# Kernel optimization log

Measured on AMD Instinct MI355X. Metric: run time of the kernel, lower is better.

## Reference

```python
import jax, jax.numpy as jnp
import numpy as np
from jax import lax

SIGMA = 4
TOPK = 9
GRID = 28          # patch grid hardcoded in AnomalyMapGenerator
IMG = 224          # input_size
SCALE = IMG // GRID  # nearest-neighbor upsample factor = 8
KSIZE = 2 * int(4.0 * SIGMA + 0.5) + 1  # 33, as in compute_anomaly_map


def _gaussian_kernel1d():
    x = jnp.arange(KSIZE, dtype=jnp.float32) - KSIZE // 2
    g = jnp.exp(-(x * x) / (2.0 * SIGMA * SIGMA))
    return g / jnp.sum(g)


def _gaussian_blur2d(x):
    # x: [B,1,H,W]; separable gaussian with reflect padding (kornia default)
    g = _gaussian_kernel1d()
    pad = KSIZE // 2
    # blur along H
    xh = jnp.pad(x, ((0, 0), (0, 0), (pad, pad), (0, 0)), mode='reflect')
    xh = lax.conv_general_dilated(xh, g.reshape(1, 1, KSIZE, 1), (1, 1), 'VALID')
    # blur along W
    xw = jnp.pad(xh, ((0, 0), (0, 0), (0, 0), (pad, pad)), mode='reflect')
    return lax.conv_general_dilated(xw, g.reshape(1, 1, 1, KSIZE), (1, 1), 'VALID')


def setup_inputs() -> dict:
    key = jax.random.key(0)
    k1, k2 = jax.random.split(key)
    embedding = jax.random.normal(k1, (3136, 1536), dtype=jnp.float32)
    memory_bank = jax.random.normal(k2, (20000, 1536), dtype=jnp.float32)  # M x D
    return {"embedding": embedding, "memory_bank": memory_bank}


def reference(embedding, memory_bank):
    x2 = jnp.sum(embedding * embedding, axis=-1, keepdims=True)        # [N,1]
    y2 = jnp.sum(memory_bank * memory_bank, axis=-1)                   # [M]
    d2 = x2 + y2[None, :] - 2.0 * (embedding @ memory_bank.T)          # [N,M]
    dist = jnp.sqrt(jnp.maximum(d2, 0.0))
    # topk smallest, ascending (matches torch.topk largest=False)
    neg_top, _ = lax.top_k(-dist, TOPK)
    patch_scores = -neg_top                                            # [N,9]

    # --- compute_anomaly_map ---
    batch = patch_scores.shape[0] // (GRID * GRID)
    amap = patch_scores[:, 0].reshape(batch, 1, GRID, GRID)
    # F.interpolate default mode='nearest' with integer factor 8 == repeat
    amap = jnp.repeat(jnp.repeat(amap, SCALE, axis=2), SCALE, axis=3)  # [B,1,224,224]
    amap = _gaussian_blur2d(amap)

    # --- compute_anomaly_score ---
    idx = jnp.argmax(patch_scores[:, 0])
    confidence = patch_scores[idx]                                     # [9]
    e = jnp.exp(confidence)
    weights = 1.0 - jnp.max(e) / jnp.sum(e)
    score = weights * jnp.max(patch_scores[:, 0])
    return amap, score
```

## Files before the change

### kernel.cpp

```cpp
#include <hip/hip_runtime.h>

typedef __attribute__((ext_vector_type(4))) int i32x4;

#define N_ROWS 3136
#define M_COLS 20000
#define KDIM   1536
#define NCT    157
#define NRT    25
#define NWG    (NCT * NRT)
#define PPR    (NCT*9)

#define QSCL   (4.0f / 127.0f)
#define QINV   (127.0f / 4.0f)
#define TWO_S2 (2.0f * QSCL * QSCL)

#define GLOAD_LDS16(g, l) __builtin_amdgcn_global_load_lds( \
    (const __attribute__((address_space(1))) unsigned int*)(g), \
    (__attribute__((address_space(3))) unsigned int*)(l), 16, 0, 0)

__device__ inline void t9_insert(float (&t)[9], float v) {
    #pragma unroll
    for (int s = 8; s >= 1; --s)
        t[s] = __builtin_amdgcn_fmed3f(v, t[s-1], t[s]);
    t[0] = fminf(t[0], v);
}

__device__ inline int q8(float x) {
    int q = (int)rintf(x * QINV);
    q = q > 127 ? 127 : q;
    q = q < -127 ? -127 : q;
    return q & 255;
}

__global__ void cvt_norm_kernel(const float* __restrict__ emb,
                                const float* __restrict__ mb,
                                unsigned char* __restrict__ embq,
                                unsigned char* __restrict__ mbq,
                                float* __restrict__ x2, float* __restrict__ y2) {
    int lane = threadIdx.x & 63;
    int row = blockIdx.x * (blockDim.x >> 6) + (threadIdx.x >> 6);
    const float* src; unsigned char* dst; float* nrm; int r;
    if (row < M_COLS) { src = mb;  dst = mbq;  nrm = y2; r = row; }
    else              { src = emb; dst = embq; nrm = x2; r = row - M_COLS; }
    const float4* p = (const float4*)(src + (size_t)r * KDIM);
    int* q = (int*)(dst + (size_t)r * KDIM);
    float s = 0.f;
    #pragma unroll
    for (int i = 0; i < 6; ++i) {
        float4 v = p[lane + i * 64];
        s += v.x*v.x + v.y*v.y + v.z*v.z + v.w*v.w;
        q[lane + i * 64] = q8(v.x) | (q8(v.y) << 8) | (q8(v.z) << 16) | (q8(v.w) << 24);
    }
    #pragma unroll
    for (int off = 32; off > 0; off >>= 1) s += __shfl_down(s, off);
    if (lane == 0) nrm[r] = s;
}

union SMem {
    unsigned char stg[2][16384];
    struct { float Ds[32 * 129]; float T9[8 * 32 * 9]; } epi;
};

#define STAGE(BUF, KT) do { \
    const int koff_ = (KT) * 64; \
    GLOAD_LDS16(pa[0] + koff_, sm.stg[BUF] + ldsoff[0]); \
    GLOAD_LDS16(pa[1] + koff_, sm.stg[BUF] + ldsoff[1]); \
    GLOAD_LDS16(pb[0] + koff_, sm.stg[BUF] + 8192 + ldsoff[0]); \
    GLOAD_LDS16(pb[1] + koff_, sm.stg[BUF] + 8192 + ldsoff[1]); \
} while (0)

#define KSTEP(CB, NB, KT, PF) do { \
    if (PF) STAGE(NB, (KT) + 1); \
    i32x4 af[4], bfr[4]; \
    _Pragma("unroll") \
    for (int mi = 0; mi < 4; ++mi) \
        af[mi] = *(const i32x4*)(sm.stg[CB] + (wr + mi * 16 + l15) * 64 + kbs); \
    _Pragma("unroll") \
    for (int ni = 0; ni < 4; ++ni) \
        bfr[ni] = *(const i32x4*)(sm.stg[CB] + 8192 + (wc + ni * 16 + l15) * 64 + kbs); \
    _Pragma("unroll") \
    for (int mi = 0; mi < 4; ++mi) \
        _Pragma("unroll") \
        for (int ni = 0; ni < 4; ++ni) \
            acc[mi][ni] = __builtin_amdgcn_mfma_i32_16x16x64_i8(af[mi], bfr[ni], acc[mi][ni], 0, 0, 0); \
    asm volatile("s_waitcnt vmcnt(0)" ::: "memory"); \
    __builtin_amdgcn_s_barrier(); \
} while (0)

__global__ __launch_bounds__(256, 4) void dist_topk_kernel(
    const unsigned char* __restrict__ Aq,
    const unsigned char* __restrict__ Bq,
    const float* __restrict__ x2, const float* __restrict__ y2,
    float* __restrict__ partials)
{
    __shared__ __align__(16) SMem sm;

    const int tid = threadIdx.x;
    const int wave = tid >> 6, lane = tid & 63;

    int orig = blockIdx.x;
    int xcd = orig & 7, li = orig >> 3;
    const int qc = NWG / 8, rc = NWG % 8;
    int wg = (xcd < rc ? xcd * (qc + 1) : rc * (qc + 1) + (xcd - rc) * qc) + li;
    const int ct = wg / NRT, rt = wg % NRT;
    const int rowBase = rt * 128, colBase = ct * 128;

    const unsigned char* pa[2];
    const unsigned char* pb[2];
    int ldsoff[2];
    #pragma unroll
    for (int i = 0; i < 2; ++i) {
        int flat = i * 256 + tid;
        int r = flat >> 2;
        int kk = (((flat & 3) ^ ((flat >> 3) & 3))) * 16;
        int ar = rowBase + r; ar = ar < N_ROWS ? ar : N_ROWS - 1;
        int bc = colBase + r; bc = bc < M_COLS ? bc : M_COLS - 1;
        pa[i] = Aq + (size_t)ar * KDIM + kk;
        pb[i] = Bq + (size_t)bc * KDIM + kk;
        ldsoff[i] = flat * 16;
    }

    const int l15 = lane & 15;
    const int kb = (lane >> 4) * 16;
    const int kbs = kb ^ (((l15 >> 1) & 3) << 4);
    const int g4 = (lane >> 4) * 4;
    const int wr = (wave >> 1) * 64;
    const int wc = (wave & 1) * 64;

    i32x4 acc[4][4] = {};

    STAGE(0, 0);
    asm volatile("s_waitcnt vmcnt(0)" ::: "memory");
    __builtin_amdgcn_s_barrier();

    #pragma unroll 1
    for (int kt = 0; kt < 24; kt += 2) {
        KSTEP(0, 1, kt, 1);
        KSTEP(1, 0, kt + 1, (kt + 2) < 24);
    }

    int ncols = M_COLS - colBase; ncols = ncols < 128 ? ncols : 128;

    #pragma unroll
    for (int p = 0; p < 4; ++p) {
        __syncthreads();
        if ((wave >> 1) == (p >> 1)) {
            const int mi0 = (p & 1) * 2;
            #pragma unroll
            for (int ni = 0; ni < 4; ++ni) {
                int c = wc + ni * 16 + l15;
                int gc = colBase + c;
                float yv = y2[gc < M_COLS ? gc : M_COLS - 1];
                #pragma unroll
                for (int mh = 0; mh < 2; ++mh) {
                    #pragma unroll
                    for (int j = 0; j < 4; ++j) {
                        int rloc = mh * 16 + g4 + j;
                        int gr = rowBase + p * 32 + rloc;
                        float xv = x2[gr < N_ROWS ? gr : N_ROWS - 1];
                        sm.epi.Ds[rloc * 129 + c] = xv + yv - TWO_S2 * (float)acc[mi0 + mh][ni][j];
                    }
                }
            }
        }
        __syncthreads();
        int r = tid & 31, q8g = tid >> 5;
        int grow = rowBase + p * 32 + r;
        float t9[9];
        #pragma unroll
        for (int s = 0; s < 9; ++s) t9[s] = 3.4e38f;
        int cs = q8g * 16;
        int ce = (cs + 16 < ncols) ? cs + 16 : ncols;
        for (int c = cs; c < ce; ++c) t9_insert(t9, sm.epi.Ds[r * 129 + c]);
        #pragma unroll
        for (int s = 0; s < 9; ++s) sm.epi.T9[(q8g * 32 + r) * 9 + s] = t9[s];
        __syncthreads();
        if (q8g < 4) {
            #pragma unroll
            for (int s = 0; s < 9; ++s)
                t9_insert(t9, sm.epi.T9[((q8g + 4) * 32 + r) * 9 + s]);
            #pragma unroll
            for (int s = 0; s < 9; ++s) sm.epi.T9[(q8g * 32 + r) * 9 + s] = t9[s];
        }
        __syncthreads();
        if (q8g == 0 && grow < N_ROWS) {
            #pragma unroll
            for (int qq = 1; qq < 4; ++qq)
                #pragma unroll
                for (int s = 0; s < 9; ++s)
                    t9_insert(t9, sm.epi.T9[(qq * 32 + r) * 9 + s]);
            float* dst = partials + (size_t)grow * PPR + ct * 9;
            #pragma unroll
            for (int s = 0; s < 9; ++s) dst[s] = t9[s];
        }
    }
}

__global__ void merge_topk_kernel(const float* __restrict__ partials,
                                  float* __restrict__ scores) {
    int lane = threadIdx.x & 63;
    int row = blockIdx.x * 4 + (threadIdx.x >> 6);
    const float* p = partials + (size_t)row * PPR;
    float t9[9];
    #pragma unroll
    for (int s = 0; s < 9; ++s) t9[s] = 3.4e38f;
    for (int i = lane; i < PPR; i += 64) {
        float v = p[i];
        if (v < t9[8]) t9_insert(t9, v);
    }
    #pragma unroll
    for (int off = 32; off > 0; off >>= 1) {
        float o[9];
        #pragma unroll
        for (int s = 0; s < 9; ++s) o[s] = __shfl_xor(t9[s], off);
        #pragma unroll
        for (int s = 0; s < 9; ++s)
            if (o[s] < t9[8]) t9_insert(t9, o[s]);
    }
    if (lane == 0) {
        #pragma unroll
        for (int s = 0; s < 9; ++s)
            scores[row * 9 + s] = sqrtf(fmaxf(t9[s], 0.f));
    }
}

__global__ void blur_h_kernel(const float* __restrict__ scores, float* __restrict__ tH) {
    int idx = blockIdx.x * blockDim.x + threadIdx.x;
    if (idx >= 4 * 224 * 28) return;
    int pw = idx % 28, y = (idx / 28) % 224, b = idx / (28 * 224);
    float acc = 0.f, gsum = 0.f;
    #pragma unroll
    for (int k = 0; k < 33; ++k) {
        float xk = (float)(k - 16);
        float w = expf(-xk * xk * (1.0f / 32.0f));
        gsum += w;
        int yy = y - 16 + k;
        yy = yy < 0 ? -yy : yy;
        yy = yy > 223 ? 446 - yy : yy;
        acc += w * scores[(size_t)(b * 784 + (yy >> 3) * 28 + pw) * 9];
    }
    tH[idx] = acc / gsum;
}

__global__ void blur_w_kernel(const float* __restrict__ tH, float* __restrict__ out) {
    int idx = blockIdx.x * blockDim.x + threadIdx.x;
    if (idx >= 4 * 224 * 224) return;
    int x = idx % 224, y = (idx / 224) % 224, b = idx / (224 * 224);
    float acc = 0.f, gsum = 0.f;
    #pragma unroll
    for (int k = 0; k < 33; ++k) {
        float xk = (float)(k - 16);
        float w = expf(-xk * xk * (1.0f / 32.0f));
        gsum += w;
        int xx = x - 16 + k;
        xx = xx < 0 ? -xx : xx;
        xx = xx > 223 ? 446 - xx : xx;
        acc += w * tH[(b * 224 + y) * 28 + (xx >> 3)];
    }
    out[idx] = acc / gsum;
}

__global__ void score_kernel(const float* __restrict__ scores, float* __restrict__ out) {
    __shared__ float vmax[256];
    __shared__ int   vidx[256];
    int tid = threadIdx.x;
    float best = -3.4e38f; int bi = 0x7fffffff;
    for (int r = tid; r < N_ROWS; r += 256) {
        float v = scores[r * 9];
        if (v > best) { best = v; bi = r; }
    }
    vmax[tid] = best; vidx[tid] = bi;
    __syncthreads();
    for (int s = 128; s > 0; s >>= 1) {
        if (tid < s) {
            if (vmax[tid + s] > vmax[tid] ||
                (vmax[tid + s] == vmax[tid] && vidx[tid + s] < vidx[tid])) {
                vmax[tid] = vmax[tid + s]; vidx[tid] = vidx[tid + s];
            }
        }
        __syncthreads();
    }
    if (tid == 0) {
        int idx = vidx[0];
        float es = 0.f, em = -3.4e38f;
        #pragma unroll
        for (int s = 0; s < 9; ++s) {
            float e = expf(scores[idx * 9 + s]);
            es += e; em = fmaxf(em, e);
        }
        out[4 * 224 * 224] = (1.0f - em / es) * vmax[0];
    }
}

extern "C" void kernel_launch(void* const* d_in, const int* in_sizes, int n_in,
                              void* d_out, int out_size, void* d_ws, size_t ws_size,
                              hipStream_t stream) {
    const float* emb = (const float*)d_in[0];
    const float* mb  = (const float*)d_in[1];
    float* out = (float*)d_out;
    char* ws = (char*)d_ws;

    unsigned char* mbq      = (unsigned char*)(ws);
    unsigned char* embq     = (unsigned char*)(ws + 30720000);
    float*         x2       = (float*)(ws + 35536896);
    float*         y2       = (float*)(ws + 35549440);
    float*         partials = (float*)(ws + 35629440);
    float*         scores   = (float*)(ws + 53354112);
    float*         tH       = (float*)(ws + 53467008);

    cvt_norm_kernel<<<(M_COLS + N_ROWS) / 4, 256, 0, stream>>>(emb, mb, embq, mbq, x2, y2);
    dist_topk_kernel<<<NWG, 256, 0, stream>>>(embq, mbq, x2, y2, partials);
    merge_topk_kernel<<<N_ROWS / 4, 256, 0, stream>>>(partials, scores);
    blur_h_kernel<<<(4 * 224 * 28 + 255) / 256, 256, 0, stream>>>(scores, tH);
    blur_w_kernel<<<(4 * 224 * 224 + 255) / 256, 256, 0, stream>>>(tH, out);
    score_kernel<<<1, 256, 0, stream>>>(scores, out);
}
```

Baseline: 209.1 us.

## Load A operand fragments directly into registers, stage only B through LDS

The int8 GEMM main loop now fetches A-tile fragments straight from global memory into double-buffered registers in MFMA operand layout. Only the B tile is still staged through LDS with global_load_lds, which halves the staging buffer and the per-step LDS reads. The wait before the barrier becomes vmcnt(4), so only the LDS-bound B loads must finish while the A register loads can stay in flight. The cost is that waves sharing the same row block load A redundantly from global/L2, and register pressure rises, so launch bounds drop from 4 to 3 waves per SIMD.

```diff
diff --git a/kernel.cpp b/kernel.cpp
--- a/kernel.cpp
+++ b/kernel.cpp
@@ -57,37 +57,39 @@
 }
 
 union SMem {
-    unsigned char stg[2][16384];
+    unsigned char stg[2][8192];
     struct { float Ds[32 * 129]; float T9[8 * 32 * 9]; } epi;
 };
 
-#define STAGE(BUF, KT) do { \
+#define STAGE_B(BUF, KT) do { \
     const int koff_ = (KT) * 64; \
-    GLOAD_LDS16(pa[0] + koff_, sm.stg[BUF] + ldsoff[0]); \
-    GLOAD_LDS16(pa[1] + koff_, sm.stg[BUF] + ldsoff[1]); \
-    GLOAD_LDS16(pb[0] + koff_, sm.stg[BUF] + 8192 + ldsoff[0]); \
-    GLOAD_LDS16(pb[1] + koff_, sm.stg[BUF] + 8192 + ldsoff[1]); \
+    GLOAD_LDS16(pb[0] + koff_, sm.stg[BUF] + ldsoff[0]); \
+    GLOAD_LDS16(pb[1] + koff_, sm.stg[BUF] + ldsoff[1]); \
 } while (0)
 
-#define KSTEP(CB, NB, KT, PF) do { \
-    if (PF) STAGE(NB, (KT) + 1); \
-    i32x4 af[4], bfr[4]; \
-    _Pragma("unroll") \
-    for (int mi = 0; mi < 4; ++mi) \
-        af[mi] = *(const i32x4*)(sm.stg[CB] + (wr + mi * 16 + l15) * 64 + kbs); \
+#define KSTEP(CB, NB, AC, AN, KT, PF) do { \
+    if (PF) { \
+        STAGE_B(NB, (KT) + 1); \
+        AN[0] = *(const i32x4*)(paf0 + ((KT) + 1) * 64); \
+        AN[1] = *(const i32x4*)(paf1 + ((KT) + 1) * 64); \
+        AN[2] = *(const i32x4*)(paf2 + ((KT) + 1) * 64); \
+        AN[3] = *(const i32x4*)(paf3 + ((KT) + 1) * 64); \
+    } \
+    i32x4 bfr[4]; \
     _Pragma("unroll") \
     for (int ni = 0; ni < 4; ++ni) \
-        bfr[ni] = *(const i32x4*)(sm.stg[CB] + 8192 + (wc + ni * 16 + l15) * 64 + kbs); \
+        bfr[ni] = *(const i32x4*)(sm.stg[CB] + (wc + ni * 16 + l15) * 64 + kbs); \
     _Pragma("unroll") \
     for (int mi = 0; mi < 4; ++mi) \
         _Pragma("unroll") \
         for (int ni = 0; ni < 4; ++ni) \
-            acc[mi][ni] = __builtin_amdgcn_mfma_i32_16x16x64_i8(af[mi], bfr[ni], acc[mi][ni], 0, 0, 0); \
-    asm volatile("s_waitcnt vmcnt(0)" ::: "memory"); \
+            acc[mi][ni] = __builtin_amdgcn_mfma_i32_16x16x64_i8(AC[mi], bfr[ni], acc[mi][ni], 0, 0, 0); \
+    if (PF) { asm volatile("s_waitcnt vmcnt(4)" ::: "memory"); } \
+    else    { asm volatile("s_waitcnt vmcnt(0)" ::: "memory"); } \
     __builtin_amdgcn_s_barrier(); \
 } while (0)
 
-__global__ __launch_bounds__(256, 4) void dist_topk_kernel(
+__global__ __launch_bounds__(256, 3) void dist_topk_kernel(
     const unsigned char* __restrict__ Aq,
     const unsigned char* __restrict__ Bq,
     const float* __restrict__ x2, const float* __restrict__ y2,
@@ -105,7 +107,6 @@
     const int ct = wg / NRT, rt = wg % NRT;
     const int rowBase = rt * 128, colBase = ct * 128;
 
-    const unsigned char* pa[2];
     const unsigned char* pb[2];
     int ldsoff[2];
     #pragma unroll
@@ -113,9 +114,7 @@
         int flat = i * 256 + tid;
         int r = flat >> 2;
         int kk = (((flat & 3) ^ ((flat >> 3) & 3))) * 16;
-        int ar = rowBase + r; ar = ar < N_ROWS ? ar : N_ROWS - 1;
         int bc = colBase + r; bc = bc < M_COLS ? bc : M_COLS - 1;
-        pa[i] = Aq + (size_t)ar * KDIM + kk;
         pb[i] = Bq + (size_t)bc * KDIM + kk;
         ldsoff[i] = flat * 16;
     }
@@ -127,16 +126,31 @@
     const int wr = (wave >> 1) * 64;
     const int wc = (wave & 1) * 64;
 
+    auto aptr = [&](int mi) {
+        int r = rowBase + wr + mi * 16 + l15;
+        r = r < N_ROWS ? r : N_ROWS - 1;
+        return Aq + (size_t)r * KDIM + kb;
+    };
+    const unsigned char* paf0 = aptr(0);
+    const unsigned char* paf1 = aptr(1);
+    const unsigned char* paf2 = aptr(2);
+    const unsigned char* paf3 = aptr(3);
+
     i32x4 acc[4][4] = {};
-
-    STAGE(0, 0);
-    asm volatile("s_waitcnt vmcnt(0)" ::: "memory");
+    i32x4 a0[4], a1[4];
+
+    STAGE_B(0, 0);
+    a0[0] = *(const i32x4*)(paf0);
+    a0[1] = *(const i32x4*)(paf1);
+    a0[2] = *(const i32x4*)(paf2);
+    a0[3] = *(const i32x4*)(paf3);
+    asm volatile("s_waitcnt vmcnt(4)" ::: "memory");
     __builtin_amdgcn_s_barrier();
 
     #pragma unroll 1
     for (int kt = 0; kt < 24; kt += 2) {
-        KSTEP(0, 1, kt, 1);
-        KSTEP(1, 0, kt + 1, (kt + 2) < 24);
+        KSTEP(0, 1, a0, a1, kt, 1);
+        KSTEP(1, 0, a1, a0, kt + 1, (kt + 2) < 24);
     }
 
     int ncols = M_COLS - colBase; ncols = ncols < 128 ? ncols : 128;
```

Measured after the change: 290.5 us. 38.9% more time.
